# Kernel tuning notes

Measured on AMD Instinct MI355X. Metric: run time of the kernel, lower is better.

## Reference

```python
import jax, jax.numpy as jnp
import numpy as np

C = 256  # image_channels == mask_channels == output_channels

def setup_inputs() -> dict:
    key = jax.random.key(0)
    ks = jax.random.split(key, 10)
    B, H, W = 16, 48, 48
    s = 0.02
    return {
        "image_feat": jax.random.normal(ks[0], (B, C, H, W), jnp.float32),
        "mask_feat": jax.random.normal(ks[1], (B, C, H, W), jnp.float32),
        "Wq": jax.random.normal(ks[2], (C, C), jnp.float32) * s,
        "bq": jnp.zeros((C,), jnp.float32),
        "Wk": jax.random.normal(ks[3], (C, C), jnp.float32) * s,
        "bk": jnp.zeros((C,), jnp.float32),
        "Wv": jax.random.normal(ks[4], (C, C), jnp.float32) * s,
        "bv": jnp.zeros((C,), jnp.float32),
        "Wo": jax.random.normal(ks[5], (C, C), jnp.float32) * s,
        "bo": jnp.zeros((C,), jnp.float32),
    }

def reference(image_feat, mask_feat, Wq, bq, Wk, bk, Wv, bv, Wo, bo):
    B, Cc, H, W = image_feat.shape
    N = H * W
    img = image_feat.reshape(B, Cc, N)   # [B, C, N]
    msk = mask_feat.reshape(B, Cc, N)
    # 1x1 convs == per-pixel linear over channels
    q = jnp.einsum('oc,bcn->bon', Wq, msk) + bq[None, :, None]
    k = jnp.einsum('oc,bcn->bon', Wk, img) + bk[None, :, None]
    v = jnp.einsum('oc,bcn->bon', Wv, img) + bv[None, :, None]
    scale = Cc ** (-0.5)
    # attn[b, n, m] = <q[:, n], k[:, m]>
    attn = jnp.einsum('bcn,bcm->bnm', q, k) * scale
    attn = jax.nn.softmax(attn, axis=-1)
    # attended[b, c, n] = sum_m v[b, c, m] * attn[b, n, m]
    av = jnp.einsum('bcm,bnm->bcn', v, attn)
    out = jnp.einsum('oc,bcn->bon', Wo, av) + bo[None, :, None]
    return image_feat + out.reshape(B, Cc, H, W)
```

## Files before the change

kernel.cpp:

```cpp
#include <hip/hip_runtime.h>

#define NBATCH 16
#define CCH 256
#define NTOK 2304

typedef __attribute__((ext_vector_type(8))) short bf16x8;
typedef __attribute__((ext_vector_type(4))) short bf16x4v;
typedef __attribute__((ext_vector_type(4))) float f32x4;

__device__ __forceinline__ short f2bf(float x){
  unsigned u = __builtin_bit_cast(unsigned, x);
  u = u + 0x7FFFu + ((u >> 16) & 1u);
  return (short)(u >> 16);
}

__device__ __forceinline__ void gld_lds16(const short* g, short* l){
  __builtin_amdgcn_global_load_lds((const __attribute__((address_space(1))) void*)g,
                                   (__attribute__((address_space(3))) void*)l, 16, 0, 0);
}

__global__ __launch_bounds__(256) void cw_kernel(const float* __restrict__ Wq, const float* __restrict__ Wk,
                                                 const float* __restrict__ Wv, const float* __restrict__ Wo,
                                                 short* __restrict__ out){
  int idx = blockIdx.x * 256 + threadIdx.x;
  int which = idx >> 14;
  int off = idx & 16383;
  const float* src = which==0 ? Wq : which==1 ? Wk : which==2 ? Wv : Wo;
  float4 v = ((const float4*)src)[off];
  bf16x4v pk = { f2bf(v.x), f2bf(v.y), f2bf(v.z), f2bf(v.w) };
  *(bf16x4v*)(out + ((size_t)which << 16) + ((size_t)off << 2)) = pk;
}

__global__ __launch_bounds__(256) void prep_kernel(const float* __restrict__ img, const float* __restrict__ msk,
                                                   short* __restrict__ imgT, short* __restrict__ mskT){
  int zz = blockIdx.z; int b = zz >> 1; int which = zz & 1;
  const float* src = (which ? msk : img) + (size_t)b * CCH * NTOK;
  short* dst = (which ? mskT : imgT) + (size_t)b * NTOK * CCH;
  int n0 = blockIdx.x * 64, c0 = blockIdx.y * 64;
  __shared__ __align__(16) short tile[64][72];
  int tid = threadIdx.x;
  int r = tid >> 2, g = tid & 3;
  const float* p = src + (size_t)(c0 + r) * NTOK + n0 + 16 * g;
  #pragma unroll
  for (int q4 = 0; q4 < 4; q4++){
    float4 v = *(const float4*)(p + 4 * q4);
    tile[16*g + 4*q4 + 0][r] = f2bf(v.x);
    tile[16*g + 4*q4 + 1][r] = f2bf(v.y);
    tile[16*g + 4*q4 + 2][r] = f2bf(v.z);
    tile[16*g + 4*q4 + 3][r] = f2bf(v.w);
  }
  __syncthreads();
  short* qp = dst + (size_t)(n0 + r) * CCH + c0 + 16 * g;
  *(bf16x8*)qp = *(const bf16x8*)&tile[r][16*g];
  *(bf16x8*)(qp + 8) = *(const bf16x8*)&tile[r][16*g + 8];
}

__device__ __forceinline__ void gemm128(const short* __restrict__ Ablk, const short* __restrict__ Bblk,
                                        short* As, short* Bs, f32x4 (&acc)[4][4]){
  const int tid = threadIdx.x;
  const int l = tid & 63, w = tid >> 6;
  const int l15 = l & 15, lhi = l >> 4;
  const int wi = w >> 1, wj = w & 1;
  const int srow = tid >> 3, scs = tid & 7;
  const f32x4 z4 = {0.f, 0.f, 0.f, 0.f};
  #pragma unroll
  for (int mt = 0; mt < 4; mt++)
    #pragma unroll
    for (int nt = 0; nt < 4; nt++) acc[mt][nt] = z4;

  #pragma unroll 1
  for (int kt = 0; kt < 4; kt++){
    const int k0 = kt * 64;
    bf16x8 ra[4], rb[4];
    #pragma unroll
    for (int p = 0; p < 4; p++){
      const int row = p * 32 + srow;
      ra[p] = *(const bf16x8*)(Ablk + (size_t)row * CCH + k0 + 8 * scs);
      rb[p] = *(const bf16x8*)(Bblk + (size_t)row * CCH + k0 + 8 * scs);
    }
    __syncthreads();
    #pragma unroll
    for (int p = 0; p < 4; p++){
      const int row = p * 32 + srow;
      const int sw = (scs ^ (row & 7)) << 3;
      *(bf16x8*)(As + row * 64 + sw) = ra[p];
      *(bf16x8*)(Bs + row * 64 + sw) = rb[p];
    }
    __syncthreads();
    #pragma unroll
    for (int kk = 0; kk < 2; kk++){
      bf16x8 afr[4], bfr[4];
      #pragma unroll
      for (int mt = 0; mt < 4; mt++){
        const int row = 64 * wi + 16 * mt + l15;
        const int ch = 4 * kk + lhi;
        afr[mt] = *(const bf16x8*)(As + row * 64 + ((ch ^ (row & 7)) << 3));
      }
      #pragma unroll
      for (int nt = 0; nt < 4; nt++){
        const int row = 64 * wj + 16 * nt + l15;
        const int ch = 4 * kk + lhi;
        bfr[nt] = *(const bf16x8*)(Bs + row * 64 + ((ch ^ (row & 7)) << 3));
      }
      #pragma unroll
      for (int mt = 0; mt < 4; mt++)
        #pragma unroll
        for (int nt = 0; nt < 4; nt++)
          acc[mt][nt] = __builtin_amdgcn_mfma_f32_16x16x32_bf16(afr[mt], bfr[nt], acc[mt][nt], 0, 0, 0);
    }
  }
}

__global__ __launch_bounds__(256) void proj_kernel(const short* __restrict__ imgT, const short* __restrict__ mskT,
                                                   const short* __restrict__ Wb,
                                                   const float* __restrict__ bq, const float* __restrict__ bk,
                                                   const float* __restrict__ bv,
                                                   short* __restrict__ Qt, short* __restrict__ Kt,
                                                   short* __restrict__ Vn){
  __shared__ __align__(16) short As[128 * 64];
  __shared__ __align__(16) short Bs[128 * 64];
  const int b = blockIdx.z, which = blockIdx.y, bx = blockIdx.x;
  const size_t nbT = (size_t)b * NTOK * CCH;
  const short* Ablk; const short* Bblk; short* outp; const float* bias;
  int ti, tj, ldout; bool biasRow; float scl;
  if (which == 0){
    ti = bx >> 1; tj = bx & 1;
    Ablk = mskT + nbT + (size_t)ti * 128 * CCH;
    Bblk = Wb + (size_t)tj * 128 * CCH;
    outp = Qt + nbT; bias = bq; ldout = CCH; biasRow = false;
    scl = 0.0625f * 1.44269504088896f;
  } else if (which == 1){
    ti = bx >> 1; tj = bx & 1;
    Ablk = imgT + nbT + (size_t)ti * 128 * CCH;
    Bblk = Wb + 65536 + (size_t)tj * 128 * CCH;
    outp = Kt + nbT; bias = bk; ldout = CCH; biasRow = false; scl = 1.0f;
  } else {
    ti = bx / 18; tj = bx % 18;
    Ablk = Wb + 2 * 65536 + (size_t)ti * 128 * CCH;
    Bblk = imgT + nbT + (size_t)tj * 128 * CCH;
    outp = Vn + nbT; bias = bv; ldout = NTOK; biasRow = true; scl = 1.0f;
  }
  f32x4 acc[4][4];
  gemm128(Ablk, Bblk, As, Bs, acc);
  const int l = threadIdx.x & 63, w = threadIdx.x >> 6;
  const int l15 = l & 15, lhi = l >> 4, wi = w >> 1, wj = w & 1;
  #pragma unroll
  for (int mt = 0; mt < 4; mt++){
    const int i0 = ti * 128 + 64 * wi + 16 * mt + 4 * lhi;
    #pragma unroll
    for (int nt = 0; nt < 4; nt++){
      const int j = tj * 128 + 64 * wj + 16 * nt + l15;
      const float bj = biasRow ? 0.f : bias[j];
      #pragma unroll
      for (int r = 0; r < 4; r++){
        float v = acc[mt][nt][r] + (biasRow ? bias[i0 + r] : bj);
        outp[(size_t)(i0 + r) * ldout + j] = f2bf(v * scl);
      }
    }
  }
}

__global__ __launch_bounds__(256) void attn_kernel(const short* __restrict__ Qt, const short* __restrict__ Kt,
                                                   const short* __restrict__ Vn, short* __restrict__ avT){
  const int phys = blockIdx.x;
  const int L = (phys & 7) * 72 + (phys >> 3);
  const int b = L / 36;
  const int q0 = (L % 36) * 64;
  const int tid = threadIdx.x, w = tid >> 6, l = tid & 63;
  const int l15 = l & 15, lhi = l >> 4;
  const short* Qb = Qt + (size_t)b * NTOK * CCH;
  const short* Kb = Kt + (size_t)b * NTOK * CCH;
  const short* Vb = Vn + (size_t)b * CCH * NTOK;
  __shared__ __align__(16) short Ks[64 * 256];
  __shared__ __align__(16) short P_lds[64][72];
  __shared__ __align__(16) float lsum_lds[64];

  const int st_row = (l >> 5);
  const int st_ch  = (l & 31);

  bf16x8 qf[8];
  {
    const short* qrow = Qb + (size_t)(q0 + 16 * w + l15) * CCH + 8 * lhi;
    #pragma unroll
    for (int kk = 0; kk < 8; kk++) qf[kk] = *(const bf16x8*)(qrow + 32 * kk);
  }
  const f32x4 z4 = {0.f, 0.f, 0.f, 0.f};
  f32x4 oacc[4][4];
  #pragma unroll
  for (int qt = 0; qt < 4; qt++)
    #pragma unroll
    for (int ct = 0; ct < 4; ct++) oacc[qt][ct] = z4;
  float lpart[4] = {0.f, 0.f, 0.f, 0.f};

#define STAGE_K(M0) do { \
    _Pragma("unroll") \
    for (int r = 0; r < 8; r++){ \
      const int slot = 4 * r + w; \
      const int row = 2 * slot + st_row; \
      const int ch = st_ch ^ (row & 7); \
      gld_lds16(Kb + (size_t)((M0) + row) * CCH + (ch << 3), &Ks[slot * 512]); \
    } } while(0)

  STAGE_K(0);

  #pragma unroll 1
  for (int t = 0; t < 36; t++){
    const int m0 = t * 64;
    __syncthreads();

    bf16x8 vfp[8];
    #pragma unroll
    for (int km = 0; km < 2; km++)
      #pragma unroll
      for (int ct = 0; ct < 4; ct++)
        vfp[4 * km + ct] = *(const bf16x8*)(Vb + (size_t)(64 * w + 16 * ct + l15) * NTOK + m0 + 32 * km + 8 * lhi);

    f32x4 sacc[4] = {z4, z4, z4, z4};
    __builtin_amdgcn_s_setprio(1);
    #pragma unroll
    for (int mjb = 0; mjb < 4; mjb++){
      const int row = 16 * mjb + l15;
      const int rsw = row & 7;
      #pragma unroll
      for (int kk = 0; kk < 8; kk++){
        bf16x8 kf = *(const bf16x8*)(Ks + row * 256 + (((4 * kk + lhi) ^ rsw) << 3));
        sacc[mjb] = __builtin_amdgcn_mfma_f32_16x16x32_bf16(qf[kk], kf, sacc[mjb], 0, 0, 0);
      }
    }
    __builtin_amdgcn_s_setprio(0);
    #pragma unroll
    for (int mjb = 0; mjb < 4; mjb++)
      #pragma unroll
      for (int r = 0; r < 4; r++){
        float p = exp2f(sacc[mjb][r]);
        lpart[r] += p;
        P_lds[16 * w + 4 * lhi + r][16 * mjb + l15] = f2bf(p);
      }
    __syncthreads();

    if (t + 1 < 36) STAGE_K(m0 + 64);

    __builtin_amdgcn_s_setprio(1);
    #pragma unroll
    for (int km = 0; km < 2; km++){
      bf16x8 pf[4];
      #pragma unroll
      for (int qt = 0; qt < 4; qt++)
        pf[qt] = *(const bf16x8*)&P_lds[16 * qt + l15][32 * km + 8 * lhi];
      #pragma unroll
      for (int qt = 0; qt < 4; qt++)
        #pragma unroll
        for (int ct = 0; ct < 4; ct++)
          oacc[qt][ct] = __builtin_amdgcn_mfma_f32_16x16x32_bf16(pf[qt], vfp[4 * km + ct], oacc[qt][ct], 0, 0, 0);
    }
    __builtin_amdgcn_s_setprio(0);
  }
#undef STAGE_K

  #pragma unroll
  for (int r = 0; r < 4; r++){
    float s = lpart[r];
    s += __shfl_xor(s, 1); s += __shfl_xor(s, 2); s += __shfl_xor(s, 4); s += __shfl_xor(s, 8);
    if (l15 == 0) lsum_lds[16 * w + 4 * lhi + r] = s;
  }
  __syncthreads();
  short* avb = avT + (size_t)b * NTOK * CCH;
  #pragma unroll
  for (int qt = 0; qt < 4; qt++){
    f32x4 lv = *(const f32x4*)&lsum_lds[16 * qt + 4 * lhi];
    f32x4 inv;
    #pragma unroll
    for (int r = 0; r < 4; r++) inv[r] = 1.0f / lv[r];
    #pragma unroll
    for (int ct = 0; ct < 4; ct++)
      #pragma unroll
      for (int r = 0; r < 4; r++)
        avb[(size_t)(q0 + 16 * qt + 4 * lhi + r) * CCH + 64 * w + 16 * ct + l15] =
            f2bf(oacc[qt][ct][r] * inv[r]);
  }
}

__global__ __launch_bounds__(256) void final_kernel(const short* __restrict__ Wb, const short* __restrict__ avT,
                                                    const float* __restrict__ bo, const float* __restrict__ img,
                                                    float* __restrict__ out){
  __shared__ __align__(16) short As[128 * 64];
  __shared__ __align__(16) short Bs[128 * 64];
  const int b = blockIdx.y, bx = blockIdx.x;
  const int ti = bx / 18, tj = bx % 18;
  const short* Ablk = Wb + 3 * 65536 + (size_t)ti * 128 * CCH;
  const short* Bblk = avT + (size_t)b * NTOK * CCH + (size_t)tj * 128 * CCH;
  f32x4 acc[4][4];
  gemm128(Ablk, Bblk, As, Bs, acc);
  const int l = threadIdx.x & 63, w = threadIdx.x >> 6;
  const int l15 = l & 15, lhi = l >> 4, wi = w >> 1, wj = w & 1;
  const float* imgb = img + (size_t)b * CCH * NTOK;
  float* outb = out + (size_t)b * CCH * NTOK;
  #pragma unroll
  for (int mt = 0; mt < 4; mt++){
    const int i0 = ti * 128 + 64 * wi + 16 * mt + 4 * lhi;
    #pragma unroll
    for (int nt = 0; nt < 4; nt++){
      const int j = tj * 128 + 64 * wj + 16 * nt + l15;
      #pragma unroll
      for (int r = 0; r < 4; r++){
        const size_t idx = (size_t)(i0 + r) * NTOK + j;
        outb[idx] = acc[mt][nt][r] + bo[i0 + r] + imgb[idx];
      }
    }
  }
}

extern "C" void kernel_launch(void* const* d_in, const int* in_sizes, int n_in,
                              void* d_out, int out_size, void* d_ws, size_t ws_size,
                              hipStream_t stream) {
  const float* img = (const float*)d_in[0];
  const float* msk = (const float*)d_in[1];
  const float* Wq  = (const float*)d_in[2];
  const float* bq  = (const float*)d_in[3];
  const float* Wk  = (const float*)d_in[4];
  const float* bk  = (const float*)d_in[5];
  const float* Wv  = (const float*)d_in[6];
  const float* bv  = (const float*)d_in[7];
  const float* Wo  = (const float*)d_in[8];
  const float* bo  = (const float*)d_in[9];
  float* out = (float*)d_out;

  short* ws = (short*)d_ws;
  const size_t NE = (size_t)NBATCH * NTOK * CCH;
  short* imgT = ws;
  short* mskT = ws + NE;
  short* Qt   = ws + 2 * NE;
  short* Kt   = ws + 3 * NE;
  short* Vn   = ws + 4 * NE;
  short* Wb   = ws + 5 * NE;
  short* avT  = mskT;

  cw_kernel<<<dim3(256), dim3(256), 0, stream>>>(Wq, Wk, Wv, Wo, Wb);
  prep_kernel<<<dim3(36, 4, 32), dim3(256), 0, stream>>>(img, msk, imgT, mskT);
  proj_kernel<<<dim3(36, 3, 16), dim3(256), 0, stream>>>(imgT, mskT, Wb, bq, bk, bv, Qt, Kt, Vn);
  attn_kernel<<<dim3(576), dim3(256), 0, stream>>>(Qt, Kt, Vn, avT);
  final_kernel<<<dim3(36, 16), dim3(256), 0, stream>>>(Wb, avT, bo, img, out);
}
```

Measured before the change: 277.1 us.

## Prefetch V fragments a tile ahead and swizzle P tile in LDS

Moves the V register loads to the end of the previous iteration so they overlap the next QK^T phase. The full __syncthreads calls are replaced with explicit waitcnt plus s_barrier: the first waits on vmcnt(8), leaving the eight newest V loads in flight while the K tile is ready. The P tile drops its padding in favour of an XOR swizzle to avoid bank conflicts, and the lsum buffer reuses P's LDS. The hand-counted vmcnt makes correctness depend on exact load ordering, and holding V across the loop raises register pressure.

```diff
diff --git a/kernel.cpp b/kernel.cpp
--- a/kernel.cpp
+++ b/kernel.cpp
@@ -172,8 +172,7 @@
   const short* Kb = Kt + (size_t)b * NTOK * CCH;
   const short* Vb = Vn + (size_t)b * CCH * NTOK;
   __shared__ __align__(16) short Ks[64 * 256];
-  __shared__ __align__(16) short P_lds[64][72];
-  __shared__ __align__(16) float lsum_lds[64];
+  __shared__ __align__(16) short P_lds[64 * 64];
 
   const int st_row = (l >> 5);
   const int st_ch  = (l & 31);
@@ -201,19 +200,25 @@
       gld_lds16(Kb + (size_t)((M0) + row) * CCH + (ch << 3), &Ks[slot * 512]); \
     } } while(0)
 
+#define LOAD_V(VFP, M0) do { \
+    _Pragma("unroll") \
+    for (int km = 0; km < 2; km++) \
+      _Pragma("unroll") \
+      for (int ct = 0; ct < 4; ct++) \
+        VFP[4*km+ct] = *(const bf16x8*)(Vb + (size_t)(64*w + 16*ct + l15) * NTOK + (M0) + 32*km + 8*lhi); \
+    } while(0)
+
+  bf16x8 vfp[8];
   STAGE_K(0);
+  LOAD_V(vfp, 0);
 
   #pragma unroll 1
   for (int t = 0; t < 36; t++){
     const int m0 = t * 64;
-    __syncthreads();
-
-    bf16x8 vfp[8];
-    #pragma unroll
-    for (int km = 0; km < 2; km++)
-      #pragma unroll
-      for (int ct = 0; ct < 4; ct++)
-        vfp[4 * km + ct] = *(const bf16x8*)(Vb + (size_t)(64 * w + 16 * ct + l15) * NTOK + m0 + 32 * km + 8 * lhi);
+    asm volatile("s_waitcnt vmcnt(8)" ::: "memory");
+    __builtin_amdgcn_sched_barrier(0);
+    __builtin_amdgcn_s_barrier();
+    __builtin_amdgcn_sched_barrier(0);
 
     f32x4 sacc[4] = {z4, z4, z4, z4};
     __builtin_amdgcn_s_setprio(1);
@@ -234,9 +239,14 @@
       for (int r = 0; r < 4; r++){
         float p = exp2f(sacc[mjb][r]);
         lpart[r] += p;
-        P_lds[16 * w + 4 * lhi + r][16 * mjb + l15] = f2bf(p);
-      }
-    __syncthreads();
+        const int prow = 16 * w + 4 * lhi + r;
+        const int pcol = 16 * mjb + l15;
+        P_lds[prow * 64 + ((((pcol >> 3) ^ (prow & 7)) << 3) | (pcol & 7))] = f2bf(p);
+      }
+    asm volatile("s_waitcnt lgkmcnt(0)" ::: "memory");
+    __builtin_amdgcn_sched_barrier(0);
+    __builtin_amdgcn_s_barrier();
+    __builtin_amdgcn_sched_barrier(0);
 
     if (t + 1 < 36) STAGE_K(m0 + 64);
 
@@ -245,8 +255,10 @@
     for (int km = 0; km < 2; km++){
       bf16x8 pf[4];
       #pragma unroll
-      for (int qt = 0; qt < 4; qt++)
-        pf[qt] = *(const bf16x8*)&P_lds[16 * qt + l15][32 * km + 8 * lhi];
+      for (int qt = 0; qt < 4; qt++){
+        const int prow = 16 * qt + l15;
+        pf[qt] = *(const bf16x8*)&P_lds[prow * 64 + (((4 * km + lhi) ^ (prow & 7)) << 3)];
+      }
       #pragma unroll
       for (int qt = 0; qt < 4; qt++)
         #pragma unroll
@@ -254,9 +266,14 @@
           oacc[qt][ct] = __builtin_amdgcn_mfma_f32_16x16x32_bf16(pf[qt], vfp[4 * km + ct], oacc[qt][ct], 0, 0, 0);
     }
     __builtin_amdgcn_s_setprio(0);
+
+    if (t + 1 < 36) LOAD_V(vfp, m0 + 64);
   }
 #undef STAGE_K
-
+#undef LOAD_V
+
+  __syncthreads();
+  float* lsum_lds = (float*)P_lds;
   #pragma unroll
   for (int r = 0; r < 4; r++){
     float s = lpart[r];
```

Result: slower. 376.3 us (+35.8%).

## Split attention key range across two blocks and add a reduction kernel

Applied to the files above, without the earlier changes.

The attention kernel now splits each query tile's 36 key tiles into two halves handled by separate blocks, doubling the grid from 576 to 1152. Each half writes its unnormalized bf16 partial output and row sums, and a new reduce kernel combines them, normalizes, and writes avT. The P_lds buffer also drops its padded layout for an XOR-swizzled one to avoid bank conflicts. The aim is better CU occupancy and load balance, at the cost of an extra kernel launch, extra global traffic, and an added bf16 rounding of the partials, which are stored in the output buffer as scratch.

```diff
diff --git a/kernel.cpp b/kernel.cpp
--- a/kernel.cpp
+++ b/kernel.cpp
@@ -12,6 +12,10 @@
   unsigned u = __builtin_bit_cast(unsigned, x);
   u = u + 0x7FFFu + ((u >> 16) & 1u);
   return (short)(u >> 16);
+}
+__device__ __forceinline__ float bf2f(short h){
+  unsigned u = ((unsigned)(unsigned short)h) << 16;
+  return __builtin_bit_cast(float, u);
 }
 
 __device__ __forceinline__ void gld_lds16(const short* g, short* l){
@@ -161,19 +165,22 @@
 }
 
 __global__ __launch_bounds__(256) void attn_kernel(const short* __restrict__ Qt, const short* __restrict__ Kt,
-                                                   const short* __restrict__ Vn, short* __restrict__ avT){
+                                                   const short* __restrict__ Vn,
+                                                   short* __restrict__ Opart, float* __restrict__ lsumg){
   const int phys = blockIdx.x;
-  const int L = (phys & 7) * 72 + (phys >> 3);
-  const int b = L / 36;
-  const int q0 = (L % 36) * 64;
+  const int L = (phys & 7) * 144 + (phys >> 3);
+  const int b = L / 72;
+  const int rem = L % 72;
+  const int half = rem / 36;
+  const int q0 = (rem % 36) * 64;
+  const int t0 = half * 18;
   const int tid = threadIdx.x, w = tid >> 6, l = tid & 63;
   const int l15 = l & 15, lhi = l >> 4;
   const short* Qb = Qt + (size_t)b * NTOK * CCH;
   const short* Kb = Kt + (size_t)b * NTOK * CCH;
   const short* Vb = Vn + (size_t)b * CCH * NTOK;
   __shared__ __align__(16) short Ks[64 * 256];
-  __shared__ __align__(16) short P_lds[64][72];
-  __shared__ __align__(16) float lsum_lds[64];
+  __shared__ __align__(16) short P_lds[64 * 64];
 
   const int st_row = (l >> 5);
   const int st_ch  = (l & 31);
@@ -201,10 +208,10 @@
       gld_lds16(Kb + (size_t)((M0) + row) * CCH + (ch << 3), &Ks[slot * 512]); \
     } } while(0)
 
-  STAGE_K(0);
+  STAGE_K(t0 * 64);
 
   #pragma unroll 1
-  for (int t = 0; t < 36; t++){
+  for (int t = t0; t < t0 + 18; t++){
     const int m0 = t * 64;
     __syncthreads();
 
@@ -234,19 +241,23 @@
       for (int r = 0; r < 4; r++){
         float p = exp2f(sacc[mjb][r]);
         lpart[r] += p;
-        P_lds[16 * w + 4 * lhi + r][16 * mjb + l15] = f2bf(p);
+        const int prow = 16 * w + 4 * lhi + r;
+        const int pcol = 16 * mjb + l15;
+        P_lds[prow * 64 + ((((pcol >> 3) ^ (prow & 7)) << 3) | (pcol & 7))] = f2bf(p);
       }
     __syncthreads();
 
-    if (t + 1 < 36) STAGE_K(m0 + 64);
+    if (t + 1 < t0 + 18) STAGE_K(m0 + 64);
 
     __builtin_amdgcn_s_setprio(1);
     #pragma unroll
     for (int km = 0; km < 2; km++){
       bf16x8 pf[4];
       #pragma unroll
-      for (int qt = 0; qt < 4; qt++)
-        pf[qt] = *(const bf16x8*)&P_lds[16 * qt + l15][32 * km + 8 * lhi];
+      for (int qt = 0; qt < 4; qt++){
+        const int prow = 16 * qt + l15;
+        pf[qt] = *(const bf16x8*)&P_lds[prow * 64 + (((4 * km + lhi) ^ (prow & 7)) << 3)];
+      }
       #pragma unroll
       for (int qt = 0; qt < 4; qt++)
         #pragma unroll
@@ -257,27 +268,37 @@
   }
 #undef STAGE_K
 
+  const size_t hrow = ((size_t)half * NBATCH + b) * NTOK + q0;
   #pragma unroll
   for (int r = 0; r < 4; r++){
     float s = lpart[r];
     s += __shfl_xor(s, 1); s += __shfl_xor(s, 2); s += __shfl_xor(s, 4); s += __shfl_xor(s, 8);
-    if (l15 == 0) lsum_lds[16 * w + 4 * lhi + r] = s;
-  }
-  __syncthreads();
-  short* avb = avT + (size_t)b * NTOK * CCH;
-  #pragma unroll
-  for (int qt = 0; qt < 4; qt++){
-    f32x4 lv = *(const f32x4*)&lsum_lds[16 * qt + 4 * lhi];
-    f32x4 inv;
-    #pragma unroll
-    for (int r = 0; r < 4; r++) inv[r] = 1.0f / lv[r];
+    if (l15 == 0) lsumg[hrow + 16 * w + 4 * lhi + r] = s;
+  }
+  short* Ob = Opart + hrow * CCH;
+  #pragma unroll
+  for (int qt = 0; qt < 4; qt++)
     #pragma unroll
     for (int ct = 0; ct < 4; ct++)
       #pragma unroll
       for (int r = 0; r < 4; r++)
-        avb[(size_t)(q0 + 16 * qt + 4 * lhi + r) * CCH + 64 * w + 16 * ct + l15] =
-            f2bf(oacc[qt][ct][r] * inv[r]);
-  }
+        Ob[(size_t)(16 * qt + 4 * lhi + r) * CCH + 64 * w + 16 * ct + l15] = f2bf(oacc[qt][ct][r]);
+}
+
+__global__ __launch_bounds__(256) void reduce_kernel(const short* __restrict__ Op, const float* __restrict__ ls,
+                                                     short* __restrict__ avT){
+  const size_t HSZ = (size_t)NBATCH * NTOK * CCH;
+  int idx = blockIdx.x * 256 + threadIdx.x;
+  int row = idx >> 5;
+  int c0 = (idx & 31) << 3;
+  float inv = 1.0f / (ls[row] + ls[NBATCH * NTOK + row]);
+  bf16x8 a = *(const bf16x8*)(Op + (size_t)row * CCH + c0);
+  bf16x8 c = *(const bf16x8*)(Op + HSZ + (size_t)row * CCH + c0);
+  bf16x8 o;
+  #pragma unroll
+  for (int j = 0; j < 8; j++)
+    o[j] = f2bf((bf2f(a[j]) + bf2f(c[j])) * inv);
+  *(bf16x8*)(avT + (size_t)row * CCH + c0) = o;
 }
 
 __global__ __launch_bounds__(256) void final_kernel(const short* __restrict__ Wb, const short* __restrict__ avT,
@@ -333,11 +354,14 @@
   short* Kt   = ws + 3 * NE;
   short* Vn   = ws + 4 * NE;
   short* Wb   = ws + 5 * NE;
+  float* lsumg = (float*)(ws + 5 * NE + 4 * 65536);
   short* avT  = mskT;
+  short* Opart = (short*)d_out;
 
   cw_kernel<<<dim3(256), dim3(256), 0, stream>>>(Wq, Wk, Wv, Wo, Wb);
   prep_kernel<<<dim3(36, 4, 32), dim3(256), 0, stream>>>(img, msk, imgT, mskT);
   proj_kernel<<<dim3(36, 3, 16), dim3(256), 0, stream>>>(imgT, mskT, Wb, bq, bk, bv, Qt, Kt, Vn);
-  attn_kernel<<<dim3(576), dim3(256), 0, stream>>>(Qt, Kt, Vn, avT);
+  attn_kernel<<<dim3(1152), dim3(256), 0, stream>>>(Qt, Kt, Vn, Opart, lsumg);
+  reduce_kernel<<<dim3(4608), dim3(256), 0, stream>>>(Opart, lsumg, avT);
   final_kernel<<<dim3(36, 16), dim3(256), 0, stream>>>(Wb, avT, bo, img, out);
 }
```

New measurement: 250.2 us. 1.11x faster.
